# Performance work log

Hardware: AMD Instinct MI355X
Metric: run time of the kernel (lower is better)

## Reference

```python
import jax, jax.numpy as jnp
import numpy as np

EPS = 1e-5
B, C_IN, C_OUT, N, K = 2, 8, 128, 65536, 16


def setup_inputs() -> dict:
    key = jax.random.key(0)
    ks = jax.random.split(key, 20)
    f = lambda k, shape, s=0.05: jax.random.normal(k, shape, dtype=jnp.float32) * s
    pv = lambda k, shape: jax.random.uniform(k, shape, dtype=jnp.float32) + 0.5
    return {
        "x": jax.random.normal(ks[0], (B, C_IN, N), dtype=jnp.float32),
        "neighbors": jax.random.randint(ks[1], (B, K, N), 0, N, dtype=jnp.int32),
        # BatchNorm1d (eval mode)
        "g1": pv(ks[2], (C_IN,)), "b1": f(ks[3], (C_IN,)),
        "m1": f(ks[4], (C_IN,)), "v1": pv(ks[5], (C_IN,)),
        # conv1: 1x1 Conv1d C_in -> C_out, with bias
        "w1": f(ks[6], (C_OUT, C_IN)), "c1b": f(ks[7], (C_OUT,)),
        # conv2[0]: BatchNorm2d(C_in)
        "g2": pv(ks[8], (C_IN,)), "b2": f(ks[9], (C_IN,)),
        "m2": f(ks[10], (C_IN,)), "v2": pv(ks[11], (C_IN,)),
        # conv2[1]: 1x1 Conv2d C_in -> C_out, no bias
        "wA": f(ks[12], (C_OUT, C_IN)),
        # conv2[2]: BatchNorm2d(C_out)
        "g3": pv(ks[13], (C_OUT,)), "b3": f(ks[14], (C_OUT,)),
        "m3": f(ks[15], (C_OUT,)), "v3": pv(ks[16], (C_OUT,)),
        # conv2[4]: 1x1 Conv2d C_out -> C_out, no bias
        "wB": f(ks[17], (C_OUT, C_OUT)),
        # final: 1x1 Conv1d 2*C_out -> C_out, with bias
        "wf": f(ks[18], (C_OUT, 2 * C_OUT)), "bf": f(ks[19], (C_OUT,)),
    }


def reference(x, neighbors, g1, b1, m1, v1, w1, c1b, g2, b2, m2, v2, wA,
              g3, b3, m3, v3, wB, wf, bf):
    # BatchNorm1d (eval): y = x*scale + shift, per channel
    s1 = g1 * jax.lax.rsqrt(v1 + EPS)
    xn = x * s1[None, :, None] + (b1 - m1 * s1)[None, :, None]  # (B, C_in, N)

    # per-point embedding: 1x1 conv
    point_emb = jnp.einsum('oc,bcn->bon', w1, xn) + c1b[None, :, None]  # (B, C_out, N)

    # gather neighbors 1..K-1 along point dim, subtract center point
    idx = neighbors[:, 1:, :]  # (B, K-1, N)
    gathered = jnp.take_along_axis(xn[:, :, None, :], idx[:, None, :, :], axis=3)  # (B, C_in, K-1, N)
    neigh = gathered - xn[:, :, None, :]

    # conv2: BN2d -> 1x1 conv -> BN2d -> ReLU -> 1x1 conv
    s2 = g2 * jax.lax.rsqrt(v2 + EPS)
    h = neigh * s2[None, :, None, None] + (b2 - m2 * s2)[None, :, None, None]
    h = jnp.einsum('oc,bckn->bokn', wA, h)  # (B, C_out, K-1, N)
    s3 = g3 * jax.lax.rsqrt(v3 + EPS)
    h = h * s3[None, :, None, None] + (b3 - m3 * s3)[None, :, None, None]
    h = jax.nn.relu(h)
    h = jnp.einsum('oc,bckn->bokn', wB, h)
    neigh_emb = jnp.max(h, axis=2)  # max over neighbors -> (B, C_out, N)

    cat = jnp.concatenate((point_emb, neigh_emb), axis=1)  # (B, 2*C_out, N)
    return jnp.einsum('oc,bcn->bon', wf, cat) + bf[None, :, None]
```

## Files before the change

### kernel.cpp

```cpp
#include <hip/hip_runtime.h>
#include <hip/hip_bf16.h>

typedef unsigned short u16;
typedef unsigned int u32;
typedef short bf16x8 __attribute__((ext_vector_type(8)));
typedef float f32x4 __attribute__((ext_vector_type(4)));

#define EPSV 1e-5f
#define WS_A3L   0
#define WS_WB    8192
#define WS_WCAT  40960
#define WS_XH    81920

union U4 { uint4 q; bf16x8 v; };

__device__ __forceinline__ u16 f2bf(float f) {
    union { __hip_bfloat16 h; u16 u; } cv;
    cv.h = __float2bfloat16(f);
    return cv.u;
}
__device__ __forceinline__ u32 pack_rne(float a, float b) {
    u32 ua = __float_as_uint(a), ub = __float_as_uint(b);
    ua = ua + 0x7FFFu + ((ua >> 16) & 1u);
    ub = ub + 0x7FFFu + ((ub >> 16) & 1u);
    return (ua >> 16) | (ub & 0xFFFF0000u);
}

__global__ __launch_bounds__(256) void prep_kernel(
    const float* g1, const float* b1, const float* m1, const float* v1,
    const float* w1, const float* c1b,
    const float* g2, const float* b2, const float* m2, const float* v2,
    const float* wA,
    const float* g3, const float* b3, const float* m3, const float* v3,
    const float* wB, const float* wf, const float* bfv,
    u16* A3L, u16* wBh, u16* Wc)
{
    __shared__ float wfL[16384];
    __shared__ float w1s[1024];
    __shared__ float c1s[128];
    __shared__ float s1[8], be1[8], s2[8], be2[8];
    __shared__ float w1fS[128][8];
    __shared__ float cbS[128];
    int t = threadIdx.x;

    for (int i = t; i < 16384; i += 256) wfL[i] = wf[((i >> 7) << 8) + (i & 127)];
    for (int i = t; i < 1024; i += 256) w1s[i] = w1[i];
    if (t < 128) c1s[t] = c1b[t];
    if (t < 8) {
        float s = g1[t] * rsqrtf(v1[t] + EPSV); s1[t] = s; be1[t] = b1[t] - m1[t] * s;
        float u = g2[t] * rsqrtf(v2[t] + EPSV); s2[t] = u; be2[t] = b2[t] - m2[t] * u;
    }
    __syncthreads();

    {
        int o = t >> 1, half = t & 1;
        float a0 = 0.f, a1 = 0.f, a2 = 0.f, a3 = 0.f, cb = 0.f;
        const float* wro = wfL + o * 128;
        int i0 = half * 4;
        for (int c = 0; c < 128; c++) {
            float f = wro[c];
            const float* wr = w1s + c * 8 + i0;
            a0 += f * wr[0]; a1 += f * wr[1]; a2 += f * wr[2]; a3 += f * wr[3];
            if (half) cb += f * c1s[c];
        }
        w1fS[o][i0] = a0; w1fS[o][i0 + 1] = a1; w1fS[o][i0 + 2] = a2; w1fS[o][i0 + 3] = a3;
        if (half) cbS[o] = cb;
    }
    __syncthreads();

    if (t < 128) {
        int o = t;
        float s3 = g3[o] * rsqrtf(v3[o] + EPSV);
        float be3 = b3[o] - m3[o] * s3;
        float csum = 0.f;
        #pragma unroll
        for (int i = 0; i < 8; i++) {
            float wv = wA[o * 8 + i];
            A3L[o * 32 + i] = f2bf(s3 * wv * s2[i] * s1[i]);
            csum += wv * be2[i];
        }
        A3L[o * 32 + 8] = f2bf(s3 * csum + be3);
        for (int k = 9; k < 32; k++) A3L[o * 32 + k] = 0;

        float bs = bfv[o] + cbS[o];
        #pragma unroll
        for (int i = 0; i < 8; i++) {
            float w1f = w1fS[o][i];
            bs += w1f * be1[i];
            Wc[o * 160 + 128 + i] = f2bf(w1f * s1[i]);
        }
        Wc[o * 160 + 136] = f2bf(bs);
        for (int k = 137; k < 160; k++) Wc[o * 160 + k] = 0;
    }
    for (int j = t; j < 16384; j += 256) {
        int o = j >> 7, c = j & 127;
        Wc[o * 160 + c] = f2bf(wf[o * 256 + 128 + c]);
    }
    {
        u32* wbo = (u32*)wBh;
        for (int j = t; j < 8192; j += 256)
            wbo[j] = pack_rne(wB[2 * j], wB[2 * j + 1]);
    }
}

__global__ __launch_bounds__(256) void xhat_kernel(const float* __restrict__ x,
                                                   float* __restrict__ xh)
{
    int t = blockIdx.x * 256 + threadIdx.x;
    int b = t >> 16, n = t & 65535;
    float4 a, c;
    a.x = x[(((b << 3) + 0) << 16) | n];
    a.y = x[(((b << 3) + 1) << 16) | n];
    a.z = x[(((b << 3) + 2) << 16) | n];
    a.w = x[(((b << 3) + 3) << 16) | n];
    c.x = x[(((b << 3) + 4) << 16) | n];
    c.y = x[(((b << 3) + 5) << 16) | n];
    c.z = x[(((b << 3) + 6) << 16) | n];
    c.w = x[(((b << 3) + 7) << 16) | n];
    float4* o = (float4*)xh + ((size_t)t << 1);
    o[0] = a; o[1] = c;
}

#define S1(P, BUF)                                                            \
    {                                                                         \
        U4 bfr; bfr.q = DX[(((P) << 4) + l15) * 5 + quad];                    \
        f32x4 z0 = {0.f, 0.f, 0.f, 0.f}, z1 = {0.f, 0.f, 0.f, 0.f};           \
        z0 = __builtin_amdgcn_mfma_f32_16x16x32_bf16(a3f[0], bfr.v, z0, 0, 0, 0); \
        z1 = __builtin_amdgcn_mfma_f32_16x16x32_bf16(a3f[1], bfr.v, z1, 0, 0, 0); \
        u32 w00 = pack_rne(fmaxf(z0[0], 0.f), fmaxf(z0[1], 0.f));             \
        u32 w01 = pack_rne(fmaxf(z0[2], 0.f), fmaxf(z0[3], 0.f));             \
        u32 w10 = pack_rne(fmaxf(z1[0], 0.f), fmaxf(z1[1], 0.f));             \
        u32 w11 = pack_rne(fmaxf(z1[2], 0.f), fmaxf(z1[3], 0.f));             \
        u32* ab = (u32*)Abuf + (BUF) * 1024 + (l15 << 6) + ((quad & 1) << 1); \
        int gA = ((w << 2) + (quad >> 1)) ^ (l15 & 7);                        \
        int gB = ((w << 2) + 2 + (quad >> 1)) ^ (l15 & 7);                    \
        *(uint2*)(ab + (gA << 2)) = make_uint2(w00, w01);                     \
        *(uint2*)(ab + (gB << 2)) = make_uint2(w10, w11);                     \
    }

#define S2(P, BUF)                                                            \
    {                                                                         \
        f32x4 acc0 = {0.f, 0.f, 0.f, 0.f}, acc1 = {0.f, 0.f, 0.f, 0.f};       \
        _Pragma("unroll")                                                     \
        for (int kt = 0; kt < 4; ++kt) {                                      \
            U4 a; a.q = Abuf[BUF][l15][((kt << 2) + quad) ^ (l15 & 7)];       \
            acc0 = __builtin_amdgcn_mfma_f32_16x16x32_bf16(a.v, wBf[0][kt], acc0, 0, 0, 0); \
            acc1 = __builtin_amdgcn_mfma_f32_16x16x32_bf16(a.v, wBf[1][kt], acc1, 0, 0, 0); \
        }                                                                     \
        float m0 = fmaxf(fmaxf(fmaxf(acc0[0], acc0[1]), acc0[2]), acc0[3]);   \
        float m1 = fmaxf(fmaxf(fmaxf(acc1[0], acc1[1]), acc1[2]), acc1[3]);   \
        m0 = fmaxf(m0, __shfl_xor(m0, 16, 64));                               \
        m0 = fmaxf(m0, __shfl_xor(m0, 32, 64));                               \
        m1 = fmaxf(m1, __shfl_xor(m1, 16, 64));                               \
        m1 = fmaxf(m1, __shfl_xor(m1, 32, 64));                               \
        if (l < 32)                                                           \
            NEu16[(P) * 168 + (w << 5) + l] =                                 \
                (u16)((__float_as_uint((quad == 0) ? m0 : m1) + 0x8000u) >> 16); \
    }

__global__ __launch_bounds__(256, 4) void heavy_kernel(
    const float* __restrict__ xh, const int* __restrict__ nbr,
    const u16* __restrict__ A3Lg, const u16* __restrict__ wBh,
    const u16* __restrict__ Wcat, const float* __restrict__ x,
    float* __restrict__ out)
{
    __shared__ uint4 DX[256 * 5];
    __shared__ uint4 Abuf[2][16][16];
    __shared__ uint4 NExq[16 * 21];
    u16* NEu16 = (u16*)NExq;
    int t = threadIdx.x;
    int w = t >> 6, l = t & 63;
    int quad = l >> 4, l15 = l & 15;

    bf16x8 wBf[2][4];
    #pragma unroll
    for (int j = 0; j < 2; j++)
        #pragma unroll
        for (int kt = 0; kt < 4; kt++) {
            U4 u; u.q = *(const uint4*)(wBh + (w * 32 + j * 16 + l15) * 128 + kt * 32 + quad * 8);
            wBf[j][kt] = u.v;
        }
    bf16x8 a3f[2];
    #pragma unroll
    for (int mi = 0; mi < 2; mi++) {
        U4 u; u.q = *(const uint4*)(A3Lg + (((2 * w + mi) * 16 + l15) << 5) + quad * 8);
        a3f[mi] = u.v;
    }

    int pbase = blockIdx.x << 4;
    int b = pbase >> 16;
    int n0 = pbase & 65535;

    for (int j = t; j < 336; j += 256) NExq[j] = make_uint4(0u, 0u, 0u, 0u);

    {
        int pt = t >> 4, slot = t & 15;
        int srow = (slot < 15) ? slot + 1 : 1;
        int idx = nbr[(b << 20) | (srow << 16) | (n0 + pt)];
        const float4* xq = (const float4*)xh + ((size_t)b << 17);
        float4 ga = xq[(u32)(idx << 1)], gb = xq[(u32)((idx << 1) + 1)];
        float4 ca = xq[(u32)((n0 + pt) << 1)], cb = xq[(u32)(((n0 + pt) << 1) + 1)];
        uint4 d;
        d.x = pack_rne(ga.x - ca.x, ga.y - ca.y);
        d.y = pack_rne(ga.z - ca.z, ga.w - ca.w);
        d.z = pack_rne(gb.x - cb.x, gb.y - cb.y);
        d.w = pack_rne(gb.z - cb.z, gb.w - cb.w);
        DX[t * 5 + 0] = d;
        DX[t * 5 + 1] = make_uint4(0x00003F80u, 0u, 0u, 0u);
        DX[t * 5 + 2] = make_uint4(0u, 0u, 0u, 0u);
        DX[t * 5 + 3] = make_uint4(0u, 0u, 0u, 0u);
    }
    __syncthreads();

    S1(0, 0)
    __syncthreads();

    for (int p = 0; p < 16; p += 2) {
        S1(p + 1, 1)
        S2(p, 0)
        __syncthreads();
        if (p < 14) S1(p + 2, 0)
        S2(p + 1, 1)
        __syncthreads();
    }

    if (t < 64) {
        int pt = t >> 2, pr = t & 3;
        float xa = x[((b * 8 + 2 * pr) << 16) + n0 + pt];
        float xb = x[((b * 8 + 2 * pr + 1) << 16) + n0 + pt];
        ((u32*)NExq)[pt * 84 + 64 + pr] = pack_rne(xa, xb);
        if (pr == 0) ((u32*)NExq)[pt * 84 + 68] = 0x3F80u;
    }
    __syncthreads();

    bf16x8 Wcf[2][5];
    #pragma unroll
    for (int mt = 0; mt < 2; mt++)
        #pragma unroll
        for (int kt = 0; kt < 5; kt++) {
            U4 u; u.q = *(const uint4*)(Wcat + (w * 32 + mt * 16 + l15) * 160 + kt * 32 + quad * 8);
            Wcf[mt][kt] = u.v;
        }
    f32x4 oa[2];
    oa[0] = (f32x4){0.f, 0.f, 0.f, 0.f};
    oa[1] = (f32x4){0.f, 0.f, 0.f, 0.f};
    #pragma unroll
    for (int kt = 0; kt < 5; ++kt) {
        U4 u; u.q = NExq[l15 * 21 + kt * 4 + quad];
        oa[0] = __builtin_amdgcn_mfma_f32_16x16x32_bf16(Wcf[0][kt], u.v, oa[0], 0, 0, 0);
        oa[1] = __builtin_amdgcn_mfma_f32_16x16x32_bf16(Wcf[1][kt], u.v, oa[1], 0, 0, 0);
    }
    #pragma unroll
    for (int mt = 0; mt < 2; ++mt) {
        int ob = w * 32 + mt * 16 + quad * 4;
        #pragma unroll
        for (int r = 0; r < 4; ++r)
            out[(((b << 7) + ob + r) << 16) + n0 + l15] = oa[mt][r];
    }
}

extern "C" void kernel_launch(void* const* d_in, const int* in_sizes, int n_in,
                              void* d_out, int out_size, void* d_ws, size_t ws_size,
                              hipStream_t stream) {
    const float* x   = (const float*)d_in[0];
    const int*   nbr = (const int*)d_in[1];
    const float* g1  = (const float*)d_in[2];
    const float* b1  = (const float*)d_in[3];
    const float* m1  = (const float*)d_in[4];
    const float* v1  = (const float*)d_in[5];
    const float* w1  = (const float*)d_in[6];
    const float* c1b = (const float*)d_in[7];
    const float* g2  = (const float*)d_in[8];
    const float* b2  = (const float*)d_in[9];
    const float* m2  = (const float*)d_in[10];
    const float* v2  = (const float*)d_in[11];
    const float* wA  = (const float*)d_in[12];
    const float* g3  = (const float*)d_in[13];
    const float* b3  = (const float*)d_in[14];
    const float* m3  = (const float*)d_in[15];
    const float* v3  = (const float*)d_in[16];
    const float* wB  = (const float*)d_in[17];
    const float* wf  = (const float*)d_in[18];
    const float* bfv = (const float*)d_in[19];

    u16*   A3L  = (u16*)((char*)d_ws + WS_A3L);
    u16*   wBh  = (u16*)((char*)d_ws + WS_WB);
    u16*   Wcat = (u16*)((char*)d_ws + WS_WCAT);
    float* xh   = (float*)((char*)d_ws + WS_XH);
    float* out  = (float*)d_out;

    prep_kernel<<<1, 256, 0, stream>>>(g1, b1, m1, v1, w1, c1b, g2, b2, m2, v2,
                                       wA, g3, b3, m3, v3, wB, wf, bfv, A3L, wBh, Wcat);
    xhat_kernel<<<512, 256, 0, stream>>>(x, xh);
    heavy_kernel<<<8192, 256, 0, stream>>>(xh, nbr, A3L, wBh, Wcat, x, out);
}
```

Measured before the change: 252.3 us.

## Shrink LDS staging, use hardware bf16 pack, raise occupancy target

```diff
diff --git a/kernel.cpp b/kernel.cpp
--- a/kernel.cpp
+++ b/kernel.cpp
@@ -123,14 +123,22 @@
 
 #define S1(P, BUF)                                                            \
     {                                                                         \
-        U4 bfr; bfr.q = DX[(((P) << 4) + l15) * 5 + quad];                    \
+        U4 bfr;                                                               \
+        if (quad == 0)      bfr.q = DXs[((P) << 4) + l15];                    \
+        else if (quad == 1) bfr.q = make_uint4(0x00003F80u, 0u, 0u, 0u);      \
+        else                bfr.q = make_uint4(0u, 0u, 0u, 0u);               \
         f32x4 z0 = {0.f, 0.f, 0.f, 0.f}, z1 = {0.f, 0.f, 0.f, 0.f};           \
         z0 = __builtin_amdgcn_mfma_f32_16x16x32_bf16(a3f[0], bfr.v, z0, 0, 0, 0); \
         z1 = __builtin_amdgcn_mfma_f32_16x16x32_bf16(a3f[1], bfr.v, z1, 0, 0, 0); \
-        u32 w00 = pack_rne(fmaxf(z0[0], 0.f), fmaxf(z0[1], 0.f));             \
-        u32 w01 = pack_rne(fmaxf(z0[2], 0.f), fmaxf(z0[3], 0.f));             \
-        u32 w10 = pack_rne(fmaxf(z1[0], 0.f), fmaxf(z1[1], 0.f));             \
-        u32 w11 = pack_rne(fmaxf(z1[2], 0.f), fmaxf(z1[3], 0.f));             \
+        u32 w00, w01, w10, w11;                                               \
+        asm("v_cvt_pk_bf16_f32 %0, %1, %2" : "=v"(w00)                        \
+            : "v"(fmaxf(z0[0], 0.f)), "v"(fmaxf(z0[1], 0.f)));                \
+        asm("v_cvt_pk_bf16_f32 %0, %1, %2" : "=v"(w01)                        \
+            : "v"(fmaxf(z0[2], 0.f)), "v"(fmaxf(z0[3], 0.f)));                \
+        asm("v_cvt_pk_bf16_f32 %0, %1, %2" : "=v"(w10)                        \
+            : "v"(fmaxf(z1[0], 0.f)), "v"(fmaxf(z1[1], 0.f)));                \
+        asm("v_cvt_pk_bf16_f32 %0, %1, %2" : "=v"(w11)                        \
+            : "v"(fmaxf(z1[2], 0.f)), "v"(fmaxf(z1[3], 0.f)));                \
         u32* ab = (u32*)Abuf + (BUF) * 1024 + (l15 << 6) + ((quad & 1) << 1); \
         int gA = ((w << 2) + (quad >> 1)) ^ (l15 & 7);                        \
         int gB = ((w << 2) + 2 + (quad >> 1)) ^ (l15 & 7);                    \
@@ -158,13 +166,12 @@
                 (u16)((__float_as_uint((quad == 0) ? m0 : m1) + 0x8000u) >> 16); \
     }
 
-__global__ __launch_bounds__(256, 4) void heavy_kernel(
+__global__ __launch_bounds__(256, 6) void heavy_kernel(
     const float* __restrict__ xh, const int* __restrict__ nbr,
     const u16* __restrict__ A3Lg, const u16* __restrict__ wBh,
-    const u16* __restrict__ Wcat, const float* __restrict__ x,
-    float* __restrict__ out)
+    const u16* __restrict__ Wcat, float* __restrict__ out)
 {
-    __shared__ uint4 DX[256 * 5];
+    __shared__ uint4 DXs[256];
     __shared__ uint4 Abuf[2][16][16];
     __shared__ uint4 NExq[16 * 21];
     u16* NEu16 = (u16*)NExq;
@@ -190,6 +197,7 @@
     int pbase = blockIdx.x << 4;
     int b = pbase >> 16;
     int n0 = pbase & 65535;
+    const float4* xq = (const float4*)xh + ((size_t)b << 17);
 
     for (int j = t; j < 336; j += 256) NExq[j] = make_uint4(0u, 0u, 0u, 0u);
 
@@ -197,7 +205,6 @@
         int pt = t >> 4, slot = t & 15;
         int srow = (slot < 15) ? slot + 1 : 1;
         int idx = nbr[(b << 20) | (srow << 16) | (n0 + pt)];
-        const float4* xq = (const float4*)xh + ((size_t)b << 17);
         float4 ga = xq[(u32)(idx << 1)], gb = xq[(u32)((idx << 1) + 1)];
         float4 ca = xq[(u32)((n0 + pt) << 1)], cb = xq[(u32)(((n0 + pt) << 1) + 1)];
         uint4 d;
@@ -205,10 +212,7 @@
         d.y = pack_rne(ga.z - ca.z, ga.w - ca.w);
         d.z = pack_rne(gb.x - cb.x, gb.y - cb.y);
         d.w = pack_rne(gb.z - cb.z, gb.w - cb.w);
-        DX[t * 5 + 0] = d;
-        DX[t * 5 + 1] = make_uint4(0x00003F80u, 0u, 0u, 0u);
-        DX[t * 5 + 2] = make_uint4(0u, 0u, 0u, 0u);
-        DX[t * 5 + 3] = make_uint4(0u, 0u, 0u, 0u);
+        DXs[t] = d;
     }
     __syncthreads();
 
@@ -224,12 +228,15 @@
         __syncthreads();
     }
 
-    if (t < 64) {
-        int pt = t >> 2, pr = t & 3;
-        float xa = x[((b * 8 + 2 * pr) << 16) + n0 + pt];
-        float xb = x[((b * 8 + 2 * pr + 1) << 16) + n0 + pt];
-        ((u32*)NExq)[pt * 84 + 64 + pr] = pack_rne(xa, xb);
-        if (pr == 0) ((u32*)NExq)[pt * 84 + 68] = 0x3F80u;
+    if (t < 16) {
+        const float4* xr = xq + ((u32)(n0 + t) << 1);
+        float4 xa = xr[0], xb = xr[1];
+        u32* dst = (u32*)NExq + t * 84 + 64;
+        dst[0] = pack_rne(xa.x, xa.y);
+        dst[1] = pack_rne(xa.z, xa.w);
+        dst[2] = pack_rne(xb.x, xb.y);
+        dst[3] = pack_rne(xb.z, xb.w);
+        dst[4] = 0x3F80u;
     }
     __syncthreads();
 
@@ -292,5 +299,5 @@
     prep_kernel<<<1, 256, 0, stream>>>(g1, b1, m1, v1, w1, c1b, g2, b2, m2, v2,
                                        wA, g3, b3, m3, v3, wB, wf, bfv, A3L, wBh, Wcat);
     xhat_kernel<<<512, 256, 0, stream>>>(x, xh);
-    heavy_kernel<<<8192, 256, 0, stream>>>(xh, nbr, A3L, wBh, Wcat, x, out);
-}
+    heavy_kernel<<<8192, 256, 0, stream>>>(xh, nbr, A3L, wBh, Wcat, out);
+}
```

Result: faster. 243.4 us (-3.5%).
